# Optimization experiments

Measured on AMD Instinct MI355X. Metric: run time of the kernel, lower is better.

The kernel has to match this reference:

```python
import jax, jax.numpy as jnp
import numpy as np

B, N, D, E = 4, 4096, 1024, 64
EPS = 1e-9
THRESH = 0.2            # second_threshold_eval
CAP_FACTOR = 2.0        # capacity_factor_eval
MIN_EXPERT_CAPACITY = 4


def setup_inputs() -> dict:
    key = jax.random.key(0)
    k1, k2 = jax.random.split(key)
    x = jax.random.normal(k1, (B, N, D), dtype=jnp.float32)
    w_gating = jax.random.normal(k2, (D, E), dtype=jnp.float32)
    return {"x": x, "w_gating": w_gating}


def _cumsum_exclusive(t, axis):
    # exclusive cumsum along `axis` (equivalent to pad-then-cumsum-then-slice)
    return jnp.cumsum(t, axis=axis) - t


def _gating(x, w_gating):
    b, n, d = x.shape
    e = w_gating.shape[-1]
    dt = x.dtype

    gate_logits = jnp.einsum('bnd,de->bne', x, w_gating)   # [b,n,e]
    raw_gates = jax.nn.softmax(gate_logits, axis=-1)

    index_1 = jnp.argmax(raw_gates, axis=-1)               # [b,n]
    gate_1 = jnp.max(raw_gates, axis=-1)                   # [b,n]
    mask_1 = jax.nn.one_hot(index_1, e, dtype=dt)          # [b,n,e]
    density_1_proxy = raw_gates

    gates_without_top_1 = raw_gates * (1.0 - mask_1)
    index_2 = jnp.argmax(gates_without_top_1, axis=-1)
    gate_2 = jnp.max(gates_without_top_1, axis=-1)
    mask_2 = jax.nn.one_hot(index_2, e, dtype=dt)

    denom = gate_1 + gate_2 + EPS
    gate_1 = gate_1 / denom
    gate_2 = gate_2 / denom

    # load-balancing aux loss
    density_1 = jnp.mean(mask_1, axis=-2)                  # [b,e]
    density_proxy = jnp.mean(density_1_proxy, axis=-2)     # [b,e]
    loss = jnp.mean(density_proxy * density_1) * float(e * e)

    # second-expert policy: 'threshold'
    mask_2 = mask_2 * (gate_2 > THRESH).astype(dt)[..., None]

    expert_capacity = max(min(n, int(n * CAP_FACTOR / e)), MIN_EXPERT_CAPACITY)
    cap_f = float(expert_capacity)

    # capacity routing for top-1
    position_in_expert_1 = _cumsum_exclusive(mask_1, axis=-2) * mask_1
    mask_1 = mask_1 * (position_in_expert_1 < cap_f).astype(dt)
    mask_1_count = jnp.sum(mask_1, axis=-2, keepdims=True)  # [b,1,e]
    mask_1_flat = jnp.sum(mask_1, axis=-1)                  # [b,n]
    position_in_expert_1 = jnp.sum(position_in_expert_1, axis=-1)  # [b,n]
    gate_1 = gate_1 * mask_1_flat

    # capacity routing for top-2 (offset by top-1 counts)
    position_in_expert_2 = (_cumsum_exclusive(mask_2, axis=-2) + mask_1_count) * mask_2
    mask_2 = mask_2 * (position_in_expert_2 < cap_f).astype(dt)
    mask_2_flat = jnp.sum(mask_2, axis=-1)
    position_in_expert_2 = jnp.sum(position_in_expert_2, axis=-1)
    gate_2 = gate_2 * mask_2_flat

    # one_hot with out-of-range index -> all zeros, matching safe_one_hot's clipping
    oh_e1 = jax.nn.one_hot(index_1, e, dtype=dt)
    oh_e2 = jax.nn.one_hot(index_2, e, dtype=dt)
    oh_c1 = jax.nn.one_hot(position_in_expert_1.astype(jnp.int32), expert_capacity, dtype=dt)
    oh_c2 = jax.nn.one_hot(position_in_expert_2.astype(jnp.int32), expert_capacity, dtype=dt)

    combine_tensor = (
        (gate_1 * mask_1_flat)[..., None, None] * oh_e1[..., :, None] * oh_c1[..., None, :]
        + (gate_2 * mask_2_flat)[..., None, None] * oh_e2[..., :, None] * oh_c2[..., None, :]
    )  # [b,n,e,capacity]

    router_z_loss = jnp.mean(jnp.sum(jax.nn.logsumexp(gate_logits, axis=-1), axis=-1))
    return combine_tensor, loss, router_z_loss


def reference(x, w_gating):
    combine_tensor, loss, router_z_loss = _gating(x, w_gating)
    dispatch_tensor = (combine_tensor != 0).astype(combine_tensor.dtype)
    return dispatch_tensor, combine_tensor, loss, router_z_loss
```

## Files before the change

kernel.cpp:

```cpp
#include <hip/hip_runtime.h>


#define B_DIM 4
#define N_DIM 4096
#define D_DIM 1024
#define E_DIM 64
#define CAP   128
#define NTOK  16384
#define TM    64
#define TK    64
#define GATE_BLOCKS 256
#define ZERO_BLOCKS 4096

#define WS_IDX1  0
#define WS_IDX2  65536
#define WS_G1    131072
#define WS_G2    196608
#define WS_DENS  262144
#define WS_Z     327680

__global__ __launch_bounds__(256) void fused_gating_zero(
    const float* __restrict__ x, const float* __restrict__ w,
    int* __restrict__ idx1, int* __restrict__ idx2,
    float* __restrict__ g1o, float* __restrict__ g2o,
    float* __restrict__ densPart, float* __restrict__ zPart,
    float* __restrict__ out, size_t half) {
  __shared__ __align__(16) char smem[33792];
  const int t = threadIdx.x;

  if (blockIdx.x >= GATE_BLOCKS) {
    const int zb = blockIdx.x - GATE_BLOCKS;
    float4* o4 = (float4*)out;
    const size_t base = (size_t)zb * 8192 + t;
    const float4 z = make_float4(0.f, 0.f, 0.f, 0.f);
#pragma unroll
    for (int i = 0; i < 32; ++i) o4[base + (size_t)i * 256] = z;
    if (zb == 0 && t == 0) { out[2 * half] = 0.f; out[2 * half + 1] = 0.f; }
    return;
  }

  float (*As)[68] = (float(*)[68])smem;
  float (*Bs)[64] = (float(*)[64])(smem + 17408);
  double (*Ld)[65] = (double(*)[65])smem;

  const int tokBase = blockIdx.x * TM;
  const int tok0 = 4 * (t >> 4), e0 = 4 * (t & 15);

  double acc[4][4] = {};

  for (int k0 = 0; k0 < D_DIM; k0 += TK) {
    {
      const int d4 = t & 15, rowb = t >> 4;
#pragma unroll
      for (int r = 0; r < 4; ++r) {
        float4 v = *(const float4*)(x + (size_t)(tokBase + rowb + 16 * r) * D_DIM + k0 + 4 * d4);
        *(float4*)&As[rowb + 16 * r][4 * d4] = v;
      }
      const float4* wsrc = (const float4*)(w + (size_t)k0 * E_DIM);
      float4* bdst = (float4*)&Bs[0][0];
#pragma unroll
      for (int i = 0; i < 4; ++i) bdst[t + 256 * i] = wsrc[t + 256 * i];
    }
    __syncthreads();
#pragma unroll 4
    for (int kk = 0; kk < TK; ++kk) {
      float4 bv = *(float4*)&Bs[kk][e0];
      double b0 = bv.x, b1 = bv.y, b2 = bv.z, b3 = bv.w;
      double a0 = As[tok0][kk], a1 = As[tok0 + 1][kk];
      double a2 = As[tok0 + 2][kk], a3 = As[tok0 + 3][kk];
      acc[0][0] += a0 * b0; acc[0][1] += a0 * b1; acc[0][2] += a0 * b2; acc[0][3] += a0 * b3;
      acc[1][0] += a1 * b0; acc[1][1] += a1 * b1; acc[1][2] += a1 * b2; acc[1][3] += a1 * b3;
      acc[2][0] += a2 * b0; acc[2][1] += a2 * b1; acc[2][2] += a2 * b2; acc[2][3] += a2 * b3;
      acc[3][0] += a3 * b0; acc[3][1] += a3 * b1; acc[3][2] += a3 * b2; acc[3][3] += a3 * b3;
    }
    __syncthreads();
  }

#pragma unroll
  for (int i = 0; i < 4; ++i)
#pragma unroll
    for (int j = 0; j < 4; ++j) Ld[tok0 + i][e0 + j] = acc[i][j];
  __syncthreads();

  const int wv = t >> 6, lane = t & 63;
  float densacc = 0.f, zacc = 0.f;

  for (int s = 0; s < 16; ++s) {
    const int tok = wv * 16 + s;
    const double l = Ld[tok][lane];

    double mv = l; int mi = lane;
#pragma unroll
    for (int off = 32; off; off >>= 1) {
      double ov = __shfl_xor(mv, off);
      int oi = __shfl_xor(mi, off);
      if (ov > mv || (ov == mv && oi < mi)) { mv = ov; mi = oi; }
    }
    float p = expf((float)(l - mv));
    float sum = p;
#pragma unroll
    for (int off = 32; off; off >>= 1) sum += __shfl_xor(sum, off);

    double l2 = (lane == mi) ? -1.0e300 : l;
    double mv2 = l2; int mi2 = lane;
#pragma unroll
    for (int off = 32; off; off >>= 1) {
      double ov = __shfl_xor(mv2, off);
      int oi = __shfl_xor(mi2, off);
      if (ov > mv2 || (ov == mv2 && oi < mi2)) { mv2 = ov; mi2 = oi; }
    }

    float gate1 = 1.0f / sum;
    float gate2 = expf((float)(mv2 - mv)) / sum;
    float denom = gate1 + gate2 + 1e-9f;
    float g1n = gate1 / denom, g2n = gate2 / denom;
    int i2eff = (g2n > 0.2f) ? mi2 : -1;
    float lse = (float)mv + logf(sum);

    densacc += p / sum;
    if (lane == 0) {
      const int gt = tokBase + tok;
      idx1[gt] = mi; idx2[gt] = i2eff;
      g1o[gt] = g1n; g2o[gt] = g2n;
      zacc += lse;
    }
  }

  __syncthreads();
  float* Ldns = (float*)smem;
  float* Lz = (float*)(smem + 1024);
  Ldns[wv * 64 + lane] = densacc;
  if (lane == 0) Lz[wv] = zacc;
  __syncthreads();
  if (wv == 0) {
    float d = Ldns[lane] + Ldns[64 + lane] + Ldns[128 + lane] + Ldns[192 + lane];
    densPart[(blockIdx.x << 6) + lane] = d;
    if (lane == 0) zPart[blockIdx.x] = Lz[0] + Lz[1] + Lz[2] + Lz[3];
  }
}

__global__ __launch_bounds__(256) void scan_write(
    const int* __restrict__ idx1, const int* __restrict__ idx2,
    const float* __restrict__ g1, const float* __restrict__ g2,
    const float* __restrict__ densPart, const float* __restrict__ zPart,
    float* __restrict__ out, size_t half) {
  __shared__ unsigned char posv[N_DIM];
  __shared__ float valv[N_DIM];
  __shared__ int wcnt[4];

  const int bid = blockIdx.x, b = bid >> 6, e = bid & 63;
  const int wv = threadIdx.x >> 6, lane = threadIdx.x & 63;
  const int tokBase = b * N_DIM + wv * 1024;
  const unsigned long long lmask = (1ull << lane) - 1ull;

  float* dispatch = out;

  ((int4*)posv)[threadIdx.x] = make_int4(-1, -1, -1, -1);
  __syncthreads();

  unsigned long long bal[16];

  int c = 0;
#pragma unroll
  for (int ch = 0; ch < 16; ++ch) {
    bool m = (idx1[tokBase + ch * 64 + lane] == e);
    bal[ch] = __ballot(m);
    c += __popcll(bal[ch]);
  }
  if (lane == 0) wcnt[wv] = c;
  __syncthreads();
  int pre = 0, tot = 0;
#pragma unroll
  for (int wvi = 0; wvi < 4; ++wvi) {
    int v = wcnt[wvi];
    if (wvi < wv) pre += v;
    tot += v;
  }
  int run = pre;
#pragma unroll
  for (int ch = 0; ch < 16; ++ch) {
    unsigned long long bb = bal[ch];
    if ((bb >> lane) & 1ull) {
      int p = run + __popcll(bb & lmask);
      if (p < CAP) {
        int gt = tokBase + ch * 64 + lane;
        int tl = gt - b * N_DIM;
        posv[tl] = (unsigned char)p;
        valv[tl] = g1[gt];
        dispatch[((size_t)gt * E_DIM + e) * CAP + p] = 1.0f;
      }
    }
    run += __popcll(bb);
  }
  __syncthreads();

  const int off0 = tot < CAP ? tot : CAP;
  int c2 = 0;
#pragma unroll
  for (int ch = 0; ch < 16; ++ch) {
    bool m = (idx2[tokBase + ch * 64 + lane] == e);
    bal[ch] = __ballot(m);
    c2 += __popcll(bal[ch]);
  }
  if (lane == 0) wcnt[wv] = c2;
  __syncthreads();
  int pre2 = 0;
#pragma unroll
  for (int wvi = 0; wvi < 4; ++wvi)
    if (wvi < wv) pre2 += wcnt[wvi];
  int run2 = off0 + pre2;
#pragma unroll
  for (int ch = 0; ch < 16; ++ch) {
    unsigned long long bb = bal[ch];
    if ((bb >> lane) & 1ull) {
      int p = run2 + __popcll(bb & lmask);
      if (p < CAP) {
        int gt = tokBase + ch * 64 + lane;
        int tl = gt - b * N_DIM;
        posv[tl] = (unsigned char)p;
        valv[tl] = g2[gt];
        dispatch[((size_t)gt * E_DIM + e) * CAP + p] = 1.0f;
      }
    }
    run2 += __popcll(bb);
  }

  if (wv == 0) {
    float v = densPart[(((b << 6) + lane) << 6) + e];
#pragma unroll
    for (int off = 32; off; off >>= 1) v += __shfl_xor(v, off);
    if (lane == 0)
      atomicAdd(&out[2 * half], v * (float)tot * (1.0f / 1048576.0f));
  }
  if (bid == 0 && wv == 1) {
    float v = zPart[lane] + zPart[lane + 64] + zPart[lane + 128] + zPart[lane + 192];
#pragma unroll
    for (int off = 32; off; off >>= 1) v += __shfl_xor(v, off);
    if (lane == 0) out[2 * half + 1] = v * 0.25f;
  }
  __syncthreads();

  const int grp = threadIdx.x >> 5, l = threadIdx.x & 31;
  float4* comb4 = (float4*)(out + half);
  for (int it = 0; it < 512; ++it) {
    const int tl = it * 8 + grp;
    const int pos = posv[tl];
    float4 v = make_float4(0.f, 0.f, 0.f, 0.f);
    if ((pos >> 2) == l) ((float*)&v)[pos & 3] = valv[tl];
    comb4[((size_t)(b * N_DIM + tl) * E_DIM + e) * 32 + l] = v;
  }
}

extern "C" void kernel_launch(void* const* d_in, const int* in_sizes, int n_in,
                              void* d_out, int out_size, void* d_ws, size_t ws_size,
                              hipStream_t stream) {
  const float* x = (const float*)d_in[0];
  const float* w = (const float*)d_in[1];
  float* out = (float*)d_out;
  char* ws = (char*)d_ws;

  int*   idx1 = (int*)(ws + WS_IDX1);
  int*   idx2 = (int*)(ws + WS_IDX2);
  float* g1   = (float*)(ws + WS_G1);
  float* g2   = (float*)(ws + WS_G2);
  float* densPart = (float*)(ws + WS_DENS);
  float* zPart    = (float*)(ws + WS_Z);

  const size_t half = ((size_t)out_size - 2) / 2;

  fused_gating_zero<<<GATE_BLOCKS + ZERO_BLOCKS, 256, 0, stream>>>(
      x, w, idx1, idx2, g1, g2, densPart, zPart, out, half);

  scan_write<<<B_DIM * E_DIM, 256, 0, stream>>>(idx1, idx2, g1, g2,
                                                densPart, zPart, out, half);
}
```

Before: 1.180 ms.

## Zero both output tensors in gating kernel and scatter combine values sparsely

The zero-fill blocks now clear both the dispatch and combine halves of the output with nontemporal stores. The scan kernel then scatters only the nonzero combine entries alongside the dispatch ones, instead of densely writing the whole combine tensor from shared-memory staging. This removes the second kernel's large dense write pass and its shared-memory buffers, which shortens the critical path. In exchange, the first kernel now does twice as much zeroing, and the scatter writes are uncoalesced.

```diff
diff --git a/kernel.cpp b/kernel.cpp
--- a/kernel.cpp
+++ b/kernel.cpp
@@ -10,7 +10,9 @@
 #define TM    64
 #define TK    64
 #define GATE_BLOCKS 256
-#define ZERO_BLOCKS 4096
+#define ZERO_BLOCKS 8192
+
+typedef float floatx4 __attribute__((ext_vector_type(4)));
 
 #define WS_IDX1  0
 #define WS_IDX2  65536
@@ -30,11 +32,12 @@
 
   if (blockIdx.x >= GATE_BLOCKS) {
     const int zb = blockIdx.x - GATE_BLOCKS;
-    float4* o4 = (float4*)out;
+    floatx4* o4 = (floatx4*)out;
     const size_t base = (size_t)zb * 8192 + t;
-    const float4 z = make_float4(0.f, 0.f, 0.f, 0.f);
-#pragma unroll
-    for (int i = 0; i < 32; ++i) o4[base + (size_t)i * 256] = z;
+    const floatx4 z = {0.f, 0.f, 0.f, 0.f};
+#pragma unroll
+    for (int i = 0; i < 32; ++i)
+      __builtin_nontemporal_store(z, &o4[base + (size_t)i * 256]);
     if (zb == 0 && t == 0) { out[2 * half] = 0.f; out[2 * half + 1] = 0.f; }
     return;
   }
@@ -139,25 +142,20 @@
   }
 }
 
-__global__ __launch_bounds__(256) void scan_write(
+__global__ __launch_bounds__(256) void scan_scatter(
     const int* __restrict__ idx1, const int* __restrict__ idx2,
     const float* __restrict__ g1, const float* __restrict__ g2,
     const float* __restrict__ densPart, const float* __restrict__ zPart,
     float* __restrict__ out, size_t half) {
-  __shared__ unsigned char posv[N_DIM];
-  __shared__ float valv[N_DIM];
-  __shared__ int wcnt[4];
-
-  const int bid = blockIdx.x, b = bid >> 6, e = bid & 63;
+  const int bid = blockIdx.x;
+  const int b = bid >> 6, e = bid & 63;
   const int wv = threadIdx.x >> 6, lane = threadIdx.x & 63;
   const int tokBase = b * N_DIM + wv * 1024;
   const unsigned long long lmask = (1ull << lane) - 1ull;
+  __shared__ int wcnt[4];
 
   float* dispatch = out;
-
-  ((int4*)posv)[threadIdx.x] = make_int4(-1, -1, -1, -1);
-  __syncthreads();
-
+  float* combine = out + half;
   unsigned long long bal[16];
 
   int c = 0;
@@ -183,11 +181,10 @@
     if ((bb >> lane) & 1ull) {
       int p = run + __popcll(bb & lmask);
       if (p < CAP) {
-        int gt = tokBase + ch * 64 + lane;
-        int tl = gt - b * N_DIM;
-        posv[tl] = (unsigned char)p;
-        valv[tl] = g1[gt];
-        dispatch[((size_t)gt * E_DIM + e) * CAP + p] = 1.0f;
+        int tok = tokBase + ch * 64 + lane;
+        size_t off = ((size_t)tok * E_DIM + e) * CAP + p;
+        dispatch[off] = 1.0f;
+        combine[off] = g1[tok];
       }
     }
     run += __popcll(bb);
@@ -215,11 +212,10 @@
     if ((bb >> lane) & 1ull) {
       int p = run2 + __popcll(bb & lmask);
       if (p < CAP) {
-        int gt = tokBase + ch * 64 + lane;
-        int tl = gt - b * N_DIM;
-        posv[tl] = (unsigned char)p;
-        valv[tl] = g2[gt];
-        dispatch[((size_t)gt * E_DIM + e) * CAP + p] = 1.0f;
+        int tok = tokBase + ch * 64 + lane;
+        size_t off = ((size_t)tok * E_DIM + e) * CAP + p;
+        dispatch[off] = 1.0f;
+        combine[off] = g2[tok];
       }
     }
     run2 += __popcll(bb);
@@ -237,17 +233,6 @@
 #pragma unroll
     for (int off = 32; off; off >>= 1) v += __shfl_xor(v, off);
     if (lane == 0) out[2 * half + 1] = v * 0.25f;
-  }
-  __syncthreads();
-
-  const int grp = threadIdx.x >> 5, l = threadIdx.x & 31;
-  float4* comb4 = (float4*)(out + half);
-  for (int it = 0; it < 512; ++it) {
-    const int tl = it * 8 + grp;
-    const int pos = posv[tl];
-    float4 v = make_float4(0.f, 0.f, 0.f, 0.f);
-    if ((pos >> 2) == l) ((float*)&v)[pos & 3] = valv[tl];
-    comb4[((size_t)(b * N_DIM + tl) * E_DIM + e) * 32 + l] = v;
   }
 }
 
@@ -271,6 +256,6 @@
   fused_gating_zero<<<GATE_BLOCKS + ZERO_BLOCKS, 256, 0, stream>>>(
       x, w, idx1, idx2, g1, g2, densPart, zPart, out, half);
 
-  scan_write<<<B_DIM * E_DIM, 256, 0, stream>>>(idx1, idx2, g1, g2,
-                                                densPart, zPart, out, half);
+  scan_scatter<<<B_DIM * E_DIM, 256, 0, stream>>>(idx1, idx2, g1, g2,
+                                                  densPart, zPart, out, half);
 }
```

New measurement: 1.108 ms. 6.1% less time.
